# Optimization experiments

Measured on AMD Instinct MI355X. Metric: run time of the kernel, lower is better.

The kernel has to match this reference:

```python
import jax, jax.numpy as jnp
import numpy as np

B, S, I, H, O, L = 64, 1024, 512, 512, 512, 3


def setup_inputs() -> dict:
    key = jax.random.key(0)
    ks = jax.random.split(key, 14)
    sc = 0.05  # small init to avoid gate saturation
    inp = {
        "input": jax.random.normal(ks[0], (B, S, I), jnp.float32),
        "hidden_state": jax.random.normal(ks[1], (B, L, H), jnp.float32),
        # gate params; x-side Linear has bias, h-side has none (as in torch module)
        "Wzx": jax.random.normal(ks[2], (L, I, H), jnp.float32) * sc,
        "bzx": jnp.zeros((L, H), jnp.float32),
        "Wzh": jax.random.normal(ks[3], (L, H, H), jnp.float32) * sc,
        "Wrx": jax.random.normal(ks[4], (L, I, H), jnp.float32) * sc,
        "brx": jnp.zeros((L, H), jnp.float32),
        "Wrh": jax.random.normal(ks[5], (L, H, H), jnp.float32) * sc,
        "Wgx": jax.random.normal(ks[6], (L, I, H), jnp.float32) * sc,
        "bgx": jnp.zeros((L, H), jnp.float32),
        "Wgh": jax.random.normal(ks[7], (L, H, H), jnp.float32) * sc,
        "Wout": jax.random.normal(ks[8], (H, O), jnp.float32) * sc,
        "bout": jnp.zeros((O,), jnp.float32),
    }
    return inp


def reference(input, hidden_state, Wzx, bzx, Wzh, Wrx, brx, Wrh, Wgx, bgx, Wgh, Wout, bout):
    n_layers = Wzx.shape[0]
    Bn = input.shape[0]
    Hn = hidden_state.shape[2]
    # layer_states: n_layers initial states + one extra zeros slot (matches torch code)
    states0 = jnp.concatenate(
        [jnp.transpose(hidden_state, (1, 0, 2)),
         jnp.zeros((1, Bn, Hn), input.dtype)], axis=0)  # (L+1, B, H)

    def step(states, x_t):
        x = x_t  # (B, I)
        for l in range(n_layers):
            # NOTE: faithfully reproduces the original's indexing: layer l reads
            # states[l], which for l>=1 was just overwritten by layer l-1 this step.
            h = states[l]
            z = jax.nn.sigmoid(x @ Wzx[l] + bzx[l] + h @ Wzh[l])
            r = jax.nn.sigmoid(x @ Wrx[l] + brx[l] + h @ Wrh[l])
            g = jnp.tanh(x @ Wgx[l] + bgx[l] + (r * h) @ Wgh[l])
            h = z * h + (1.0 - z) * g
            x = h  # dropout=0 -> identity
            states = states.at[l + 1].set(h)
        out_t = x @ Wout + bout  # (B, O)
        return states, out_t

    states_f, outs = jax.lax.scan(step, states0, jnp.transpose(input, (1, 0, 2)))
    layer_output = jnp.transpose(outs, (1, 0, 2))          # (B, S, O)
    hidden_out = jnp.transpose(states_f[:n_layers], (1, 0, 2))  # (B, L, H)
    return layer_output, hidden_out
```

## Files before the change

### kernel.cpp

```cpp
#include <hip/hip_runtime.h>


typedef __attribute__((ext_vector_type(4))) float f32x4;
typedef __attribute__((ext_vector_type(8))) __bf16 bf16x8;

#define NROWS 65536
#define HID_OFF 33554432ull

__device__ __forceinline__ void gload16(const void* g, void* l) {
  __builtin_amdgcn_global_load_lds((const __attribute__((address_space(1))) void*)g,
                                   (__attribute__((address_space(3))) void*)l,
                                   16, 0, 0);
}
__device__ __forceinline__ float sigmoidf_(float x) { return 1.f / (1.f + __expf(-x)); }
__device__ __forceinline__ float tanh_fast(float x) {
  const float e = __expf(2.f * x);
  return 1.f - 2.f / (e + 1.f);
}

__device__ __forceinline__ void stage32(const __bf16* __restrict__ src, int k0,
                                        __bf16* lds, int w, int lane) {
#pragma unroll
  for (int i = 0; i < 2; ++i) {
    const int s0 = (w * 2 + i) * 64;
    const int s = s0 + lane;
    const int row = s >> 2;
    const int cc = (s ^ row) & 3;
    gload16(src + (size_t)row * 512 + k0 + cc * 8, lds + s0 * 8);
  }
}

__device__ __forceinline__ bf16x8 frag32(const __bf16* t, int row, int lane) {
  const int c = ((lane >> 4) ^ row) & 3;
  return *(const bf16x8*)(t + row * 32 + c * 8);
}

__device__ __forceinline__ void stage_ht(const __bf16* __restrict__ src,
                                         __bf16* Ht, int w, int lane) {
#pragma unroll
  for (int i = 0; i < 8; ++i) {
    const int s0 = i * 256 + w * 64;
    const int s = s0 + lane;
    const int row = s >> 4, cc = s & 15;
    gload16(src + (size_t)row * 512 + cc * 8, Ht + s0 * 8);
  }
  asm volatile("s_waitcnt vmcnt(0)");
  __builtin_amdgcn_sched_barrier(0);
  __builtin_amdgcn_s_barrier();
  __builtin_amdgcn_sched_barrier(0);
}

template<int EPI, bool L0>
__global__ __launch_bounds__(256, 4) void gemm7(
    const __bf16* __restrict__ A,
    const __bf16* __restrict__ Bt,
    int tiles_n, int row_off,
    const float* __restrict__ bias,
    const float* __restrict__ cterm,
    const float* __restrict__ h0f,
    const __bf16* __restrict__ haux,
    const __bf16* __restrict__ zf,
    const __bf16* __restrict__ gf,
    __bf16* __restrict__ o_rh,
    __bf16* __restrict__ o_h,
    float* __restrict__ o_f)
{
  __shared__ alignas(16) __bf16 smem[16384];
  __bf16* const A0 = smem;
  __bf16* const B0 = smem + 4096;
  __bf16* const A1 = smem + 8192;
  __bf16* const B1 = smem + 12288;

  const int tid = threadIdx.x, lane = tid & 63, w = tid >> 6;

  int bid = blockIdx.x;
  {
    const int nwg = gridDim.x;
    const int q = nwg >> 3, r = nwg & 7;
    const int x = bid & 7, rest = bid >> 3;
    bid = (x < r ? x * (q + 1) : r * (q + 1) + (x - r) * q) + rest;
  }
  const int tm = bid / tiles_n;
  const int tn = bid - tm * tiles_n;
  const size_t arow0 = (size_t)tm * 128;
  const int brow0 = tn * 128;
  const __bf16* const Ab = A + arow0 * 512;
  const __bf16* const Bb = Bt + (size_t)brow0 * 512;

  const int wr = (w >> 1) * 64;
  const int wc = (w & 1) * 64;

  f32x4 acc[4][4];
  const f32x4 zz = {0.f, 0.f, 0.f, 0.f};
#pragma unroll
  for (int i = 0; i < 4; ++i)
#pragma unroll
    for (int j = 0; j < 4; ++j) acc[i][j] = zz;

  auto step = [&](int t, const __bf16* cA, const __bf16* cB,
                  __bf16* nA, __bf16* nB) {
    if (t < 15) {
      stage32(Ab, (t + 1) * 32, nA, w, lane);
      stage32(Bb, (t + 1) * 32, nB, w, lane);
    }
    bf16x8 af[4], bb4[4];
#pragma unroll
    for (int i = 0; i < 4; ++i) {
      af[i]  = frag32(cA, wr + i * 16 + (lane & 15), lane);
      bb4[i] = frag32(cB, wc + i * 16 + (lane & 15), lane);
    }
#pragma unroll
    for (int mi = 0; mi < 4; ++mi)
#pragma unroll
      for (int ni = 0; ni < 4; ++ni)
        acc[mi][ni] = __builtin_amdgcn_mfma_f32_16x16x32_bf16(af[mi], bb4[ni], acc[mi][ni], 0, 0, 0);
    if (t < 15) {
      asm volatile("s_waitcnt vmcnt(0)");
      __builtin_amdgcn_sched_barrier(0);
    }
    __builtin_amdgcn_sched_barrier(0);
    __builtin_amdgcn_s_barrier();
    __builtin_amdgcn_sched_barrier(0);
  };

  stage32(Ab, 0, A0, w, lane);
  stage32(Bb, 0, B0, w, lane);
  asm volatile("s_waitcnt vmcnt(0)");
  __builtin_amdgcn_sched_barrier(0);
  __builtin_amdgcn_s_barrier();
  __builtin_amdgcn_sched_barrier(0);

#pragma unroll 1
  for (int t = 0; t < 16; t += 2) {
    step(t,     A0, B0, A1, B1);
    step(t + 1, A1, B1, A0, B0);
  }

  const int fcol = lane & 15;
  const int frow = (lane >> 4) * 4;
  const int bb0 = (row_off + (int)arow0) >> 10;

  if (EPI == 0) {
    if (tn < 4) {
      const size_t foff = ((size_t)(tm * 4 + tn)) * 16384 + (size_t)tid * 64;
      __bf16* zw = (__bf16*)zf;
#pragma unroll
      for (int mi = 0; mi < 4; ++mi) {
        bf16x8 p0, p1;
#pragma unroll
        for (int ni = 0; ni < 4; ++ni)
#pragma unroll
          for (int j = 0; j < 4; ++j) {
            const int gcol = brow0 + wc + ni * 16 + fcol;
            float c = acc[mi][ni][j] + bias[gcol];
            if (L0) c += cterm[bb0 * 1024 + gcol];
            const float v = sigmoidf_(c);
            const int idx = ni * 4 + j;
            if (idx < 8) p0[idx] = (__bf16)v; else p1[idx - 8] = (__bf16)v;
          }
        *(bf16x8*)(zw + foff + mi * 16) = p0;
        *(bf16x8*)(zw + foff + mi * 16 + 8) = p1;
      }
    } else if (tn < 8) {
      if (!L0) stage_ht(haux + arow0 * 512 + (tn - 4) * 128, smem, w, lane);
#pragma unroll
      for (int mi = 0; mi < 4; ++mi)
#pragma unroll
        for (int ni = 0; ni < 4; ++ni)
#pragma unroll
          for (int j = 0; j < 4; ++j) {
            const int rloc = (int)arow0 + wr + mi * 16 + frow + j;
            const int gcol = brow0 + wc + ni * 16 + fcol;
            const int nn = gcol - 512;
            float c = acc[mi][ni][j] + bias[gcol];
            if (L0) c += cterm[bb0 * 1024 + gcol];
            const float rv = sigmoidf_(c);
            const float h = L0 ? h0f[bb0 * 1536 + nn]
                               : (float)smem[(wr + mi * 16 + frow + j) * 128 + wc + ni * 16 + fcol];
            o_rh[(size_t)rloc * 512 + nn] = (__bf16)(rv * h);
          }
    } else {
      const size_t foff = ((size_t)(tm * 4 + (tn - 8))) * 16384 + (size_t)tid * 64;
      __bf16* gw = (__bf16*)gf;
#pragma unroll
      for (int mi = 0; mi < 4; ++mi) {
        bf16x8 p0, p1;
#pragma unroll
        for (int ni = 0; ni < 4; ++ni)
#pragma unroll
          for (int j = 0; j < 4; ++j) {
            const int gcol = brow0 + wc + ni * 16 + fcol;
            const float v = acc[mi][ni][j] + bias[gcol];
            const int idx = ni * 4 + j;
            if (idx < 8) p0[idx] = (__bf16)v; else p1[idx - 8] = (__bf16)v;
          }
        *(bf16x8*)(gw + foff + mi * 16) = p0;
        *(bf16x8*)(gw + foff + mi * 16 + 8) = p1;
      }
    }
  } else if (EPI == 1) {
    if (!L0) stage_ht(haux + arow0 * 512 + tn * 128, smem, w, lane);
    const size_t foff = ((size_t)(tm * 4 + tn)) * 16384 + (size_t)tid * 64;
    const bool has_last = (o_f != nullptr) && ((tm & 7) == 7);
#pragma unroll
    for (int mi = 0; mi < 4; ++mi) {
      const bf16x8 z0 = *(const bf16x8*)(zf + foff + mi * 16);
      const bf16x8 z1 = *(const bf16x8*)(zf + foff + mi * 16 + 8);
      const bf16x8 g0 = *(const bf16x8*)(gf + foff + mi * 16);
      const bf16x8 g1 = *(const bf16x8*)(gf + foff + mi * 16 + 8);
#pragma unroll
      for (int ni = 0; ni < 4; ++ni)
#pragma unroll
        for (int j = 0; j < 4; ++j) {
          const int rloc = (int)arow0 + wr + mi * 16 + frow + j;
          const int gcol = brow0 + wc + ni * 16 + fcol;
          const int idx = ni * 4 + j;
          const float zv = (float)(idx < 8 ? z0[idx] : z1[idx - 8]);
          const float gp = (float)(idx < 8 ? g0[idx] : g1[idx - 8]);
          const float gv = tanh_fast(gp + acc[mi][ni][j]);
          const float h = L0 ? h0f[bb0 * 1536 + gcol]
                             : (float)smem[(wr + mi * 16 + frow + j) * 128 + wc + ni * 16 + fcol];
          const float hv = zv * h + (1.f - zv) * gv;
          o_h[(size_t)rloc * 512 + gcol] = (__bf16)hv;
          if (has_last && ((rloc & 1023) == 1023))
            o_f[(size_t)bb0 * 1536 + gcol] = (float)(__bf16)hv;
        }
    }
  } else {
#pragma unroll
    for (int mi = 0; mi < 4; ++mi)
#pragma unroll
      for (int ni = 0; ni < 4; ++ni)
#pragma unroll
        for (int j = 0; j < 4; ++j) {
          const int rloc = (int)arow0 + wr + mi * 16 + frow + j;
          const int gcol = brow0 + wc + ni * 16 + fcol;
          o_f[(size_t)rloc * 512 + gcol] = acc[mi][ni][j] + bias[gcol];
        }
  }
}


__global__ void prep_pack(const float* __restrict__ Wzx, const float* __restrict__ Wzh,
                          const float* __restrict__ Wrx, const float* __restrict__ Wrh,
                          const float* __restrict__ Wgx, const float* __restrict__ Wgh,
                          const float* __restrict__ Wout,
                          __bf16* __restrict__ W1t, __bf16* __restrict__ Wght,
                          __bf16* __restrict__ Woutt)
{
  const int slot = blockIdx.z;
  const float* srcA;
  const float* srcB = nullptr;
  __bf16* dst;
  if (slot < 9) {
    const int l = slot / 3, g = slot % 3;
    srcA = (g == 0 ? Wzx : g == 1 ? Wrx : Wgx) + (size_t)l * 512 * 512;
    if (l > 0 && g < 2) srcB = (g == 0 ? Wzh : Wrh) + (size_t)l * 512 * 512;
    dst = W1t + (size_t)l * 1536 * 512 + (size_t)g * 512 * 512;
  } else if (slot < 12) {
    const int l = slot - 9;
    srcA = Wgh + (size_t)l * 512 * 512;
    dst = Wght + (size_t)l * 512 * 512;
  } else {
    srcA = Wout;
    dst = Woutt;
  }
  __shared__ float tile[32][33];
  const int k0 = blockIdx.x * 32;
  const int n0 = blockIdx.y * 32;
  const int tx = threadIdx.x;
  const int ty = threadIdx.y;
  for (int i = ty; i < 32; i += 8) {
    float v = srcA[(size_t)(k0 + i) * 512 + n0 + tx];
    if (srcB) v += srcB[(size_t)(k0 + i) * 512 + n0 + tx];
    tile[i][tx] = v;
  }
  __syncthreads();
  for (int i = ty; i < 32; i += 8)
    dst[(size_t)(n0 + i) * 512 + k0 + tx] = (__bf16)tile[tx][i];
}

__global__ void cterm_kernel(const float* __restrict__ hidden,
                             const float* __restrict__ Wzh,
                             const float* __restrict__ Wrh,
                             float* __restrict__ Cterm)
{
  const int idx = blockIdx.x * blockDim.x + threadIdx.x;
  const int b = idx >> 10;
  const int n = idx & 1023;
  const float* W = (n < 512 ? Wzh : Wrh);
  const int nn = n & 511;
  const float* h0 = hidden + (size_t)b * 1536;
  float acc = 0.f;
  for (int k = 0; k < 512; ++k) acc += h0[k] * W[(size_t)k * 512 + nn];
  Cterm[idx] = acc;
}

__global__ void small_prep(const float* __restrict__ bzx, const float* __restrict__ brx,
                           const float* __restrict__ bgx, const float* __restrict__ hidden,
                           float* __restrict__ bias1, float* __restrict__ out_hidden)
{
  const int idx = blockIdx.x * blockDim.x + threadIdx.x;
  if (idx < 3 * 1536) {
    const int l = idx / 1536, j = idx % 1536;
    const float* src = (j < 512 ? bzx : j < 1024 ? brx : bgx);
    bias1[idx] = src[l * 512 + (j & 511)];
  }
  const int hidx = idx - 3 * 1536;
  if (hidx >= 0 && hidx < 64 * 512) {
    const int b = hidx >> 9, n = hidx & 511;
    out_hidden[(size_t)b * 1536 + n] = hidden[(size_t)b * 1536 + n];
  }
}

__global__ void convert_x(const float* __restrict__ src, __bf16* __restrict__ dst, long n)
{
  const long i = ((long)blockIdx.x * blockDim.x + threadIdx.x) * 8;
  if (i >= n) return;
  const f32x4 a = *(const f32x4*)(src + i);
  const f32x4 b = *(const f32x4*)(src + i + 4);
  bf16x8 o;
  o[0] = (__bf16)a[0]; o[1] = (__bf16)a[1]; o[2] = (__bf16)a[2]; o[3] = (__bf16)a[3];
  o[4] = (__bf16)b[0]; o[5] = (__bf16)b[1]; o[6] = (__bf16)b[2]; o[7] = (__bf16)b[3];
  *(bf16x8*)(dst + i) = o;
}

extern "C" void kernel_launch(void* const* d_in, const int* in_sizes, int n_in,
                              void* d_out, int out_size, void* d_ws, size_t ws_size,
                              hipStream_t stream) {
  const float* input  = (const float*)d_in[0];
  const float* hidden = (const float*)d_in[1];
  const float* Wzx = (const float*)d_in[2];
  const float* bzx = (const float*)d_in[3];
  const float* Wzh = (const float*)d_in[4];
  const float* Wrx = (const float*)d_in[5];
  const float* brx = (const float*)d_in[6];
  const float* Wrh = (const float*)d_in[7];
  const float* Wgx = (const float*)d_in[8];
  const float* bgx = (const float*)d_in[9];
  const float* Wgh = (const float*)d_in[10];
  const float* Wout = (const float*)d_in[11];
  const float* bout = (const float*)d_in[12];

  float* out = (float*)d_out;
  float* out_hidden = out + HID_OFF;

  char* ws = (char*)d_ws;
  size_t off = 0;
  auto carve = [&](size_t bytes) -> void* {
    off = (off + 255) & ~(size_t)255;
    void* p = ws + off;
    off += bytes;
    return p;
  };

  __bf16* W1t   = (__bf16*)carve(3ull * 1536 * 512 * 2);
  __bf16* Wght  = (__bf16*)carve(3ull * 512 * 512 * 2);
  __bf16* Woutt = (__bf16*)carve(512ull * 512 * 2);
  float*  bias1 = (float*) carve(3ull * 1536 * 4);
  float*  Cterm = (float*) carve(64ull * 1024 * 4);
  const size_t fixed_end = off;

  long chunk_rows = NROWS;
  int C = 1;
  while (C < 32) {
    const size_t need = ((fixed_end + 255) & ~(size_t)255) +
                        5ull * (size_t)chunk_rows * 512 * 2 + 5 * 256;
    if (need <= ws_size) break;
    C *= 2;
    chunk_rows /= 2;
  }
  __bf16* bufA  = (__bf16*)carve((size_t)chunk_rows * 512 * 2);
  __bf16* bufB  = (__bf16*)carve((size_t)chunk_rows * 512 * 2);
  __bf16* zfrag = (__bf16*)carve((size_t)chunk_rows * 512 * 2);
  __bf16* rhb   = (__bf16*)carve((size_t)chunk_rows * 512 * 2);
  __bf16* gfrag = (__bf16*)carve((size_t)chunk_rows * 512 * 2);

  small_prep<<<(3 * 1536 + 64 * 512 + 255) / 256, 256, 0, stream>>>(
      bzx, brx, bgx, hidden, bias1, out_hidden);
  dim3 tp_grid(16, 16, 13), tp_blk(32, 8);
  prep_pack<<<tp_grid, tp_blk, 0, stream>>>(Wzx, Wzh, Wrx, Wrh, Wgx, Wgh, Wout,
                                            W1t, Wght, Woutt);
  cterm_kernel<<<65536 / 256, 256, 0, stream>>>(hidden, Wzh, Wrh, Cterm);

  for (int c = 0; c < C; ++c) {
    const long row_off = (long)c * chunk_rows;
    const long nelem = chunk_rows * 512;
    const int mt = (int)(chunk_rows / 128);

    convert_x<<<(int)((nelem / 8 + 255) / 256), 256, 0, stream>>>(
        input + (size_t)row_off * 512, bufA, nelem);

    gemm7<0, true><<<mt * 12, 256, 0, stream>>>(
        bufA, W1t, 12, (int)row_off, bias1, Cterm, hidden, nullptr,
        zfrag, gfrag, rhb, nullptr, nullptr);
    gemm7<1, true><<<mt * 4, 256, 0, stream>>>(
        rhb, Wght, 4, (int)row_off, nullptr, nullptr, hidden, nullptr,
        zfrag, gfrag, nullptr, bufB, out_hidden + 512);

    gemm7<0, false><<<mt * 12, 256, 0, stream>>>(
        bufB, W1t + 1536 * 512, 12, (int)row_off, bias1 + 1536, nullptr, nullptr, bufB,
        zfrag, gfrag, rhb, nullptr, nullptr);
    gemm7<1, false><<<mt * 4, 256, 0, stream>>>(
        rhb, Wght + 512 * 512, 4, (int)row_off, nullptr, nullptr, nullptr, bufB,
        zfrag, gfrag, nullptr, bufA, out_hidden + 1024);

    gemm7<0, false><<<mt * 12, 256, 0, stream>>>(
        bufA, W1t + 2 * 1536 * 512, 12, (int)row_off, bias1 + 3072, nullptr, nullptr, bufA,
        zfrag, gfrag, rhb, nullptr, nullptr);
    gemm7<1, false><<<mt * 4, 256, 0, stream>>>(
        rhb, Wght + 2 * 512 * 512, 4, (int)row_off, nullptr, nullptr, nullptr, bufA,
        zfrag, gfrag, nullptr, bufB, nullptr);

    gemm7<2, false><<<mt * 4, 256, 0, stream>>>(
        bufB, Woutt, 4, (int)row_off, bout, nullptr, nullptr, nullptr,
        nullptr, nullptr, nullptr, nullptr, out + (size_t)row_off * 512);
  }
}
```

Measured before the change: 927.5 us.

## Change LDS swizzle, defer z sigmoid, prefetch gate fragments before staging

Changes the LDS XOR swizzle pattern for 32-wide bf16 tiles to use row>>1, aiming to cut bank conflicts on 16-byte fragment reads. It moves the z-gate sigmoid from the first GEMM epilogue into the second, so the stored bf16 value is the pre-activation. It also loads the z/g fragments into registers before the hidden-state LDS staging so their global latency overlaps that wait, and drops a redundant scheduling barrier. Storing z before the sigmoid in bf16 changes rounding, and holding the prefetched fragments raises register pressure.

```diff
diff --git a/kernel.cpp b/kernel.cpp
--- a/kernel.cpp
+++ b/kernel.cpp
@@ -25,13 +25,13 @@
     const int s0 = (w * 2 + i) * 64;
     const int s = s0 + lane;
     const int row = s >> 2;
-    const int cc = (s ^ row) & 3;
+    const int cc = ((s & 3) ^ (row >> 1)) & 3;
     gload16(src + (size_t)row * 512 + k0 + cc * 8, lds + s0 * 8);
   }
 }
 
 __device__ __forceinline__ bf16x8 frag32(const __bf16* t, int row, int lane) {
-  const int c = ((lane >> 4) ^ row) & 3;
+  const int c = (((lane >> 4) ^ (row >> 1)) & 3);
   return *(const bf16x8*)(t + row * 32 + c * 8);
 }
 
@@ -51,7 +51,7 @@
 }
 
 template<int EPI, bool L0>
-__global__ __launch_bounds__(256, 4) void gemm7(
+__global__ __launch_bounds__(256, 4) void gemm12(
     const __bf16* __restrict__ A,
     const __bf16* __restrict__ Bt,
     int tiles_n, int row_off,
@@ -97,8 +97,8 @@
 #pragma unroll
     for (int j = 0; j < 4; ++j) acc[i][j] = zz;
 
-  auto step = [&](int t, const __bf16* cA, const __bf16* cB,
-                  __bf16* nA, __bf16* nB) {
+  auto stepf = [&](int t, const __bf16* cA, const __bf16* cB,
+                   __bf16* nA, __bf16* nB) {
     if (t < 15) {
       stage32(Ab, (t + 1) * 32, nA, w, lane);
       stage32(Bb, (t + 1) * 32, nB, w, lane);
@@ -118,7 +118,6 @@
       asm volatile("s_waitcnt vmcnt(0)");
       __builtin_amdgcn_sched_barrier(0);
     }
-    __builtin_amdgcn_sched_barrier(0);
     __builtin_amdgcn_s_barrier();
     __builtin_amdgcn_sched_barrier(0);
   };
@@ -132,8 +131,8 @@
 
 #pragma unroll 1
   for (int t = 0; t < 16; t += 2) {
-    step(t,     A0, B0, A1, B1);
-    step(t + 1, A1, B1, A0, B0);
+    stepf(t,     A0, B0, A1, B1);
+    stepf(t + 1, A1, B1, A0, B0);
   }
 
   const int fcol = lane & 15;
@@ -154,9 +153,8 @@
             const int gcol = brow0 + wc + ni * 16 + fcol;
             float c = acc[mi][ni][j] + bias[gcol];
             if (L0) c += cterm[bb0 * 1024 + gcol];
-            const float v = sigmoidf_(c);
             const int idx = ni * 4 + j;
-            if (idx < 8) p0[idx] = (__bf16)v; else p1[idx - 8] = (__bf16)v;
+            if (idx < 8) p0[idx] = (__bf16)c; else p1[idx - 8] = (__bf16)c;
           }
         *(bf16x8*)(zw + foff + mi * 16) = p0;
         *(bf16x8*)(zw + foff + mi * 16 + 8) = p1;
@@ -199,15 +197,19 @@
       }
     }
   } else if (EPI == 1) {
+    const size_t foff = ((size_t)(tm * 4 + tn)) * 16384 + (size_t)tid * 64;
+    bf16x8 zr[4][2], gr[4][2];
+#pragma unroll
+    for (int mi = 0; mi < 4; ++mi) {
+      zr[mi][0] = *(const bf16x8*)(zf + foff + mi * 16);
+      zr[mi][1] = *(const bf16x8*)(zf + foff + mi * 16 + 8);
+      gr[mi][0] = *(const bf16x8*)(gf + foff + mi * 16);
+      gr[mi][1] = *(const bf16x8*)(gf + foff + mi * 16 + 8);
+    }
     if (!L0) stage_ht(haux + arow0 * 512 + tn * 128, smem, w, lane);
-    const size_t foff = ((size_t)(tm * 4 + tn)) * 16384 + (size_t)tid * 64;
     const bool has_last = (o_f != nullptr) && ((tm & 7) == 7);
 #pragma unroll
     for (int mi = 0; mi < 4; ++mi) {
-      const bf16x8 z0 = *(const bf16x8*)(zf + foff + mi * 16);
-      const bf16x8 z1 = *(const bf16x8*)(zf + foff + mi * 16 + 8);
-      const bf16x8 g0 = *(const bf16x8*)(gf + foff + mi * 16);
-      const bf16x8 g1 = *(const bf16x8*)(gf + foff + mi * 16 + 8);
 #pragma unroll
       for (int ni = 0; ni < 4; ++ni)
 #pragma unroll
@@ -215,8 +217,8 @@
           const int rloc = (int)arow0 + wr + mi * 16 + frow + j;
           const int gcol = brow0 + wc + ni * 16 + fcol;
           const int idx = ni * 4 + j;
-          const float zv = (float)(idx < 8 ? z0[idx] : z1[idx - 8]);
-          const float gp = (float)(idx < 8 ? g0[idx] : g1[idx - 8]);
+          const float zv = sigmoidf_((float)(idx < 8 ? zr[mi][0][idx] : zr[mi][1][idx - 8]));
+          const float gp = (float)(idx < 8 ? gr[mi][0][idx] : gr[mi][1][idx - 8]);
           const float gv = tanh_fast(gp + acc[mi][ni][j]);
           const float h = L0 ? h0f[bb0 * 1536 + gcol]
                              : (float)smem[(wr + mi * 16 + frow + j) * 128 + wc + ni * 16 + fcol];
@@ -391,28 +393,28 @@
     convert_x<<<(int)((nelem / 8 + 255) / 256), 256, 0, stream>>>(
         input + (size_t)row_off * 512, bufA, nelem);
 
-    gemm7<0, true><<<mt * 12, 256, 0, stream>>>(
+    gemm12<0, true><<<mt * 12, 256, 0, stream>>>(
         bufA, W1t, 12, (int)row_off, bias1, Cterm, hidden, nullptr,
         zfrag, gfrag, rhb, nullptr, nullptr);
-    gemm7<1, true><<<mt * 4, 256, 0, stream>>>(
+    gemm12<1, true><<<mt * 4, 256, 0, stream>>>(
         rhb, Wght, 4, (int)row_off, nullptr, nullptr, hidden, nullptr,
         zfrag, gfrag, nullptr, bufB, out_hidden + 512);
 
-    gemm7<0, false><<<mt * 12, 256, 0, stream>>>(
+    gemm12<0, false><<<mt * 12, 256, 0, stream>>>(
         bufB, W1t + 1536 * 512, 12, (int)row_off, bias1 + 1536, nullptr, nullptr, bufB,
         zfrag, gfrag, rhb, nullptr, nullptr);
-    gemm7<1, false><<<mt * 4, 256, 0, stream>>>(
+    gemm12<1, false><<<mt * 4, 256, 0, stream>>>(
         rhb, Wght + 512 * 512, 4, (int)row_off, nullptr, nullptr, nullptr, bufB,
         zfrag, gfrag, nullptr, bufA, out_hidden + 1024);
 
-    gemm7<0, false><<<mt * 12, 256, 0, stream>>>(
+    gemm12<0, false><<<mt * 12, 256, 0, stream>>>(
         bufA, W1t + 2 * 1536 * 512, 12, (int)row_off, bias1 + 3072, nullptr, nullptr, bufA,
         zfrag, gfrag, rhb, nullptr, nullptr);
-    gemm7<1, false><<<mt * 4, 256, 0, stream>>>(
+    gemm12<1, false><<<mt * 4, 256, 0, stream>>>(
         rhb, Wght + 2 * 512 * 512, 4, (int)row_off, nullptr, nullptr, nullptr, bufA,
         zfrag, gfrag, nullptr, bufB, nullptr);
 
-    gemm7<2, false><<<mt * 4, 256, 0, stream>>>(
+    gemm12<2, false><<<mt * 4, 256, 0, stream>>>(
         bufB, Woutt, 4, (int)row_off, bout, nullptr, nullptr, nullptr,
         nullptr, nullptr, nullptr, nullptr, out + (size_t)row_off * 512);
   }
```

Measured after the change: 931.8 us. About the same (+0.5%).
